# Performance work log

Measured on AMD Instinct MI355X. Metric: run time of the kernel, lower is better.

The kernel has to match this reference:

```python
import jax, jax.numpy as jnp
import numpy as np

B, N, C, H = 8, 1024, 768, 12
DH = C // H


def setup_inputs() -> dict:
    key = jax.random.key(0)
    k1, k2, k3, k4 = jax.random.split(key, 4)
    x = jax.random.normal(k1, (B, N, C), dtype=jnp.float32)
    mask = jax.random.randint(k2, (B, N), 0, 2, dtype=jnp.int32)
    # torch Linear weights stored transposed; build directly as (in, out)
    w_qkv = jax.random.normal(k3, (C, 3 * C), dtype=jnp.float32) * (C ** -0.5)
    w_proj = jax.random.normal(k4, (C, C), dtype=jnp.float32) * (C ** -0.5)
    b_proj = jnp.zeros((C,), dtype=jnp.float32)
    return {"x": x, "mask": mask, "w_qkv": w_qkv, "w_proj": w_proj, "b_proj": b_proj}


def reference(x, mask, w_qkv, w_proj, b_proj):
    scale = DH ** -0.5
    qkv = (x @ w_qkv).reshape(B, N, 3, H, DH)          # (B,N,3,H,Dh)
    q, k, v = jnp.moveaxis(qkv, 2, 0)                  # each (B,N,H,Dh)
    q = q.transpose(0, 2, 1, 3)                        # (B,H,N,Dh)
    k = k.transpose(0, 2, 1, 3)
    v = v.transpose(0, 2, 1, 3)
    attn = jnp.einsum('bhqd,bhkd->bhqk', q, k) * scale  # (B,H,N,N)
    # mask (B,N) masks key positions for all queries/heads
    attn = jnp.where(mask[:, None, None, :] != 0, -jnp.inf, attn)
    attn = jax.nn.softmax(attn, axis=-1)
    out = jnp.einsum('bhqk,bhkd->bhqd', attn, v)        # (B,H,N,Dh)
    out = out.transpose(0, 2, 1, 3).reshape(B, N, C)
    return out @ w_proj + b_proj
```

## Files before the change

### kernel.cpp

```cpp
#include <hip/hip_runtime.h>
#include <cstdint>
#include <cstddef>

#define Bb   8
#define Nn   1024
#define Ccn  768
#define Hh   12
#define DHn  64
#define Mrows (Bb * Nn)
#define N3C  (3 * Ccn)
#define BHn  (Bb * Hh)

typedef __attribute__((ext_vector_type(8))) short bf16x8;
typedef __attribute__((ext_vector_type(4))) float f32x4;

static __device__ __forceinline__ unsigned short f2bf(float f) {
    unsigned int u = __builtin_bit_cast(unsigned int, f);
    return (unsigned short)((u + 0x7FFFu + ((u >> 16) & 1u)) >> 16);
}
static __device__ __forceinline__ float bf2f(unsigned short s) {
    unsigned int u = ((unsigned int)s) << 16;
    return __builtin_bit_cast(float, u);
}
static __device__ __forceinline__ unsigned pack2bf(float a, float b) {
    unsigned ua = __builtin_bit_cast(unsigned, a) + 0x8000u;
    unsigned ub = __builtin_bit_cast(unsigned, b) + 0x8000u;
    return (ua >> 16) | (ub & 0xFFFF0000u);
}
static __device__ __forceinline__ void glds16(const void* g, void* l) {
    __builtin_amdgcn_global_load_lds((const __attribute__((address_space(1))) void*)g,
                                     (__attribute__((address_space(3))) void*)l,
                                     16, 0, 0);
}

__global__ void prep_kernel(const float* __restrict__ x,
                            unsigned short* __restrict__ xb,
                            const int* __restrict__ mask,
                            float* __restrict__ maskneg,
                            const float* __restrict__ Wqkv,
                            unsigned short* __restrict__ WqkvT,
                            const float* __restrict__ Wproj,
                            unsigned short* __restrict__ WprojT) {
    __shared__ float tile[32][33];
    int bx = blockIdx.x;
    if (bx < 3072) {
        int i = bx * 256 + threadIdx.x;
        if (i < Mrows) maskneg[i] = (mask[i] != 0) ? -1.0e9f : 0.0f;
        const f32x4* xp = (const f32x4*)x;
        f32x4 a = xp[2 * i], b = xp[2 * i + 1];
        bf16x8 v;
#pragma unroll
        for (int j = 0; j < 4; ++j) {
            v[j]     = (short)f2bf(a[j]);
            v[4 + j] = (short)f2bf(b[j]);
        }
        ((bf16x8*)xb)[i] = v;
        return;
    }
    bx -= 3072;
    int xt = bx % 96, yt = bx / 96;
    const float* W; unsigned short* WT; int C;
    if (xt < 72) { W = Wqkv;  WT = WqkvT;  C = N3C; }
    else         { W = Wproj; WT = WprojT; C = Ccn; xt -= 72; }
    const int R = Ccn;
    const int c0 = xt * 32, r0 = yt * 32;
    const int tx = threadIdx.x & 31, ty = threadIdx.x >> 5;
#pragma unroll
    for (int i = 0; i < 4; ++i)
        tile[ty + i * 8][tx] = W[(size_t)(r0 + ty + i * 8) * C + c0 + tx];
    __syncthreads();
#pragma unroll
    for (int i = 0; i < 4; ++i)
        WT[(size_t)(c0 + ty + i * 8) * R + r0 + tx] = f2bf(tile[tx][ty + i * 8]);
}

__global__ void transpose_v_kernel(const unsigned short* __restrict__ vb,
                                   unsigned short* __restrict__ vtb) {
    __shared__ unsigned short tile[32][34];
    const int bh = blockIdx.z;
    const int d0 = blockIdx.x * 32, n0 = blockIdx.y * 32;
    const int tx = threadIdx.x, ty = threadIdx.y;
    const unsigned short* src = vb + (size_t)bh * Nn * DHn;
    unsigned short* dst = vtb + (size_t)bh * DHn * Nn;
#pragma unroll
    for (int i = 0; i < 4; ++i)
        tile[ty + i * 8][tx] = src[(size_t)(n0 + ty + i * 8) * DHn + d0 + tx];
    __syncthreads();
#pragma unroll
    for (int i = 0; i < 4; ++i)
        dst[(size_t)(d0 + ty + i * 8) * Nn + n0 + tx] = tile[tx][ty + i * 8];
}

__global__ __launch_bounds__(256) void gemm_qkv_kernel(
    const unsigned short* __restrict__ A,
    const unsigned short* __restrict__ BT,
    unsigned short* __restrict__ qkvb) {
    constexpr int K = Ccn;
    const int bm = blockIdx.x, bn = blockIdx.y;
    const int t = threadIdx.x, wv = t >> 6, l = t & 63;
    const int fr = l & 15, quad = l >> 4;
    const int wm = (wv >> 1) * 64, wn = (wv & 1) * 64;
    __shared__ __align__(16) unsigned short As[2][128 * 32];
    __shared__ __align__(16) unsigned short Bs[2][128 * 32];
    const f32x4 zero = {0.f, 0.f, 0.f, 0.f};
    f32x4 acc[4][4];
#pragma unroll
    for (int i = 0; i < 4; ++i)
#pragma unroll
        for (int j = 0; j < 4; ++j) acc[i][j] = zero;

    const int srow = wv * 16 + (l >> 2);
    const int scol_dst = (l & 3) * 8;
    const int scol_src = (((l & 3) ^ ((srow >> 1) & 3)) << 3);
    const unsigned short* Ag = A + (size_t)(bm * 128 + srow) * K + scol_src;
    const unsigned short* Bg = BT + (size_t)(bn * 128 + srow) * K + scol_src;
    const int ldst = srow * 32 + scol_dst;
    const int rsw = ((fr >> 1) & 3);

    auto stage = [&](int r, int bsel) {
        const unsigned short* Ar = Ag + r * 32;
        const unsigned short* Br = Bg + r * 32;
        glds16(Ar, &As[bsel][ldst]);
        glds16(Ar + (size_t)64 * K, &As[bsel][ldst + 64 * 32]);
        glds16(Br, &Bs[bsel][ldst]);
        glds16(Br + (size_t)64 * K, &Bs[bsel][ldst + 64 * 32]);
    };
    stage(0, 0);
    __syncthreads();
    for (int r = 0; r < 24; ++r) {
        if (r < 23) stage(r + 1, (r + 1) & 1);
        const unsigned short* Asb = As[r & 1];
        const unsigned short* Bsb = Bs[r & 1];
        bf16x8 af[4], bfv[4];
#pragma unroll
        for (int i = 0; i < 4; ++i)
            af[i] = *(const bf16x8*)&Asb[(wm + i * 16 + fr) * 32 + ((quad ^ rsw) << 3)];
#pragma unroll
        for (int i = 0; i < 4; ++i)
            bfv[i] = *(const bf16x8*)&Bsb[(wn + i * 16 + fr) * 32 + ((quad ^ rsw) << 3)];
#pragma unroll
        for (int i = 0; i < 4; ++i)
#pragma unroll
            for (int j = 0; j < 4; ++j)
                acc[i][j] = __builtin_amdgcn_mfma_f32_16x16x32_bf16(af[i], bfv[j], acc[i][j], 0, 0, 0);
        __syncthreads();
    }
#pragma unroll
    for (int j = 0; j < 4; ++j) {
        int col = bn * 128 + wn + j * 16 + fr;
        int s = col / Ccn;
        int rem = col - s * Ccn;
        int hh = rem >> 6, d = rem & 63;
#pragma unroll
        for (int i = 0; i < 4; ++i) {
#pragma unroll
            for (int r = 0; r < 4; ++r) {
                int row = bm * 128 + wm + i * 16 + quad * 4 + r;
                int b = row >> 10, nq = row & 1023;
                qkvb[((((size_t)s * Bb + b) * Hh + hh) * Nn + nq) * DHn + d] = f2bf(acc[i][j][r]);
            }
        }
    }
}

__global__ __launch_bounds__(256) void gemm_proj_kernel(
    const unsigned short* __restrict__ A,
    const unsigned short* __restrict__ BT,
    const float* __restrict__ bias,
    float* __restrict__ out) {
    constexpr int K = Ccn;
    const int bm = blockIdx.x, bn = blockIdx.y;
    const int t = threadIdx.x, wv = t >> 6, l = t & 63;
    const int fr = l & 15, quad = l >> 4;
    const int wm = (wv >> 1) * 64, wn = (wv & 1) * 32;
    __shared__ __align__(16) unsigned short As[2][128 * 32];
    __shared__ __align__(16) unsigned short Bs[2][64 * 32];
    const f32x4 zero = {0.f, 0.f, 0.f, 0.f};
    f32x4 acc[4][2];
#pragma unroll
    for (int i = 0; i < 4; ++i)
#pragma unroll
        for (int j = 0; j < 2; ++j) acc[i][j] = zero;

    const int srow = wv * 16 + (l >> 2);
    const int scol_dst = (l & 3) * 8;
    const int scol_src = (((l & 3) ^ ((srow >> 1) & 3)) << 3);
    const unsigned short* Ag = A + (size_t)(bm * 128 + srow) * K + scol_src;
    const int ldstA = srow * 32 + scol_dst;
    const int rB = t >> 2, cB = t & 3;
    const int bsrc = ((cB ^ ((rB >> 1) & 3)) << 3);
    const unsigned short* Bg = BT + (size_t)(bn * 64 + rB) * K + bsrc;
    const int ldstB = rB * 32 + cB * 8;
    const int rsw = ((fr >> 1) & 3);

    auto stage = [&](int r, int bsel) {
        const unsigned short* Ar = Ag + r * 32;
        glds16(Ar, &As[bsel][ldstA]);
        glds16(Ar + (size_t)64 * K, &As[bsel][ldstA + 64 * 32]);
        glds16(Bg + r * 32, &Bs[bsel][ldstB]);
    };
    stage(0, 0);
    __syncthreads();
    for (int r = 0; r < 24; ++r) {
        if (r < 23) stage(r + 1, (r + 1) & 1);
        const unsigned short* Asb = As[r & 1];
        const unsigned short* Bsb = Bs[r & 1];
        bf16x8 af[4], bfv[2];
#pragma unroll
        for (int i = 0; i < 4; ++i)
            af[i] = *(const bf16x8*)&Asb[(wm + i * 16 + fr) * 32 + ((quad ^ rsw) << 3)];
#pragma unroll
        for (int j = 0; j < 2; ++j)
            bfv[j] = *(const bf16x8*)&Bsb[(wn + j * 16 + fr) * 32 + ((quad ^ rsw) << 3)];
#pragma unroll
        for (int i = 0; i < 4; ++i)
#pragma unroll
            for (int j = 0; j < 2; ++j)
                acc[i][j] = __builtin_amdgcn_mfma_f32_16x16x32_bf16(af[i], bfv[j], acc[i][j], 0, 0, 0);
        __syncthreads();
    }
#pragma unroll
    for (int j = 0; j < 2; ++j) {
        int col = bn * 64 + wn + j * 16 + fr;
        float bv = bias[col];
#pragma unroll
        for (int i = 0; i < 4; ++i) {
#pragma unroll
            for (int r = 0; r < 4; ++r) {
                int row = bm * 128 + wm + i * 16 + quad * 4 + r;
                out[(size_t)row * Ccn + col] = acc[i][j][r] + bv;
            }
        }
    }
}

__global__ __launch_bounds__(256, 3) void attn_fused(
    const unsigned short* __restrict__ qkvb,
    const unsigned short* __restrict__ vtb,
    const float* __restrict__ maskneg,
    unsigned short* __restrict__ attnb) {
    const int hb = blockIdx.x, qt = blockIdx.y;
    const int b = hb / Hh, h = hb - b * Hh;
    const int t = threadIdx.x, wv = t >> 6, l = t & 63;
    const int fr = l & 15, quad = l >> 4;
    __shared__ __align__(16) unsigned short Ks[2][64 * 64];
    __shared__ __align__(16) unsigned short VTs[2][64 * 64];
    __shared__ __align__(16) float Ms[2][64];
    __shared__ __align__(16) unsigned short Pbuf[4][16 * 72];
    const size_t bh = (size_t)b * Hh + h;
    const unsigned short* Qg = qkvb + bh * (Nn * DHn);
    const unsigned short* Kg = qkvb + (BHn + bh) * (Nn * DHn);
    const unsigned short* Vg = vtb + bh * (DHn * Nn);
    const float* Mg = maskneg + b * Nn;
    const int q0 = qt * 128 + wv * 32;

    bf16x8 qf[2][2];
#pragma unroll
    for (int g = 0; g < 2; ++g)
#pragma unroll
        for (int c = 0; c < 2; ++c) {
            bf16x8 raw = *(const bf16x8*)&Qg[(size_t)(q0 + g * 16 + fr) * DHn + c * 32 + quad * 8];
            bf16x8 sc;
#pragma unroll
            for (int j = 0; j < 8; ++j)
                sc[j] = (short)f2bf(bf2f((unsigned short)raw[j]) * 0.125f);
            qf[g][c] = sc;
        }
    const f32x4 zero = {0.f, 0.f, 0.f, 0.f};
    f32x4 o[2][4];
    float rs[2] = {0.f, 0.f};
#pragma unroll
    for (int g = 0; g < 2; ++g)
#pragma unroll
        for (int r = 0; r < 4; ++r) o[g][r] = zero;

    const int srow = wv * 8 + (l >> 3);
    const int lincol = (l & 7) * 8;
    const int swzcol = (((l & 7) ^ (srow & 7)) << 3);

    auto stage = [&](int kbase, int bsel) {
        glds16(&Kg[(size_t)(kbase + srow) * DHn + swzcol], &Ks[bsel][srow * 64 + lincol]);
        glds16(&Kg[(size_t)(kbase + srow + 32) * DHn + swzcol], &Ks[bsel][(srow + 32) * 64 + lincol]);
        glds16(&Vg[(size_t)srow * Nn + kbase + swzcol], &VTs[bsel][srow * 64 + lincol]);
        glds16(&Vg[(size_t)(srow + 32) * Nn + kbase + swzcol], &VTs[bsel][(srow + 32) * 64 + lincol]);
        if (t < 16) glds16(&Mg[kbase + t * 4], &Ms[bsel][t * 4]);
    };
    auto compute = [&](int bsel) {
        f32x4 ci[4];
#pragma unroll
        for (int kt = 0; kt < 4; ++kt)
            ci[kt] = *(const f32x4*)&Ms[bsel][kt * 16 + quad * 4];
        bf16x8 kf0[4], kf1[4];
#pragma unroll
        for (int kt = 0; kt < 4; ++kt) {
            int rr = kt * 16 + fr, sw = rr & 7;
            kf0[kt] = *(const bf16x8*)&Ks[bsel][rr * 64 + ((quad ^ sw) << 3)];
            kf1[kt] = *(const bf16x8*)&Ks[bsel][rr * 64 + (((quad + 4) ^ sw) << 3)];
        }
        f32x4 sg[2][4];
#pragma unroll
        for (int g = 0; g < 2; ++g)
#pragma unroll
            for (int kt = 0; kt < 4; ++kt) {
                f32x4 s = __builtin_amdgcn_mfma_f32_16x16x32_bf16(kf0[kt], qf[g][0], ci[kt], 0, 0, 0);
                sg[g][kt] = __builtin_amdgcn_mfma_f32_16x16x32_bf16(kf1[kt], qf[g][1], s, 0, 0, 0);
            }
        bf16x8 vf0[4], vf1[4];
#pragma unroll
        for (int dt = 0; dt < 4; ++dt) {
            int rr = dt * 16 + fr, sw = rr & 7;
            vf0[dt] = *(const bf16x8*)&VTs[bsel][rr * 64 + ((quad ^ sw) << 3)];
            vf1[dt] = *(const bf16x8*)&VTs[bsel][rr * 64 + (((quad + 4) ^ sw) << 3)];
        }
        unsigned short* Pw = Pbuf[wv];
#pragma unroll
        for (int g = 0; g < 2; ++g) {
#pragma unroll
            for (int kt = 0; kt < 4; ++kt) {
                float p0 = __expf(sg[g][kt][0]);
                float p1 = __expf(sg[g][kt][1]);
                float p2 = __expf(sg[g][kt][2]);
                float p3 = __expf(sg[g][kt][3]);
                rs[g] += (p0 + p1) + (p2 + p3);
                uint2 pk;
                pk.x = pack2bf(p0, p1);
                pk.y = pack2bf(p2, p3);
                *(uint2*)&Pw[fr * 72 + kt * 16 + quad * 4] = pk;
            }
            bf16x8 pa0 = *(const bf16x8*)&Pw[fr * 72 + quad * 8];
            bf16x8 pa1 = *(const bf16x8*)&Pw[fr * 72 + 32 + quad * 8];
#pragma unroll
            for (int dt = 0; dt < 4; ++dt) {
                f32x4 t0 = __builtin_amdgcn_mfma_f32_16x16x32_bf16(pa0, vf0[dt], o[g][dt], 0, 0, 0);
                o[g][dt] = __builtin_amdgcn_mfma_f32_16x16x32_bf16(pa1, vf1[dt], t0, 0, 0, 0);
            }
        }
    };

    stage(0, 0);
    __syncthreads();
    for (int r = 0; r < 16; ++r) {
        if (r < 15) stage((r + 1) * 64, (r + 1) & 1);
        compute(r & 1);
        __syncthreads();
    }
#pragma unroll
    for (int g = 0; g < 2; ++g) {
        float r2 = rs[g] + __shfl_xor(rs[g], 16, 64);
        float rfull = r2 + __shfl_xor(r2, 32, 64);
        float inv[4];
#pragma unroll
        for (int r = 0; r < 4; ++r) {
            float lv = __shfl(rfull, quad * 4 + r, 64);
            inv[r] = (lv > 0.f) ? 1.0f / lv : 0.f;
        }
#pragma unroll
        for (int dt = 0; dt < 4; ++dt)
#pragma unroll
            for (int r = 0; r < 4; ++r) {
                int q = q0 + g * 16 + quad * 4 + r;
                attnb[((size_t)(b * Nn + q) * Hh + h) * DHn + dt * 16 + fr] = f2bf(o[g][dt][r] * inv[r]);
            }
    }
}

#define OFF_XB     0u
#define OFF_WQKVT  12582912u
#define OFF_WPROJT 16121856u
#define OFF_MASKB  17301504u
#define OFF_QKVB   17334272u
#define OFF_VTB    55083008u
#define OFF_ATTNB  67665920u

extern "C" void kernel_launch(void* const* d_in, const int* in_sizes, int n_in,
                              void* d_out, int out_size, void* d_ws, size_t ws_size,
                              hipStream_t stream) {
    const float* x      = (const float*)d_in[0];
    const int*   mask   = (const int*)d_in[1];
    const float* w_qkv  = (const float*)d_in[2];
    const float* w_proj = (const float*)d_in[3];
    const float* b_proj = (const float*)d_in[4];
    float* out = (float*)d_out;
    char* ws = (char*)d_ws;
    unsigned short* xb     = (unsigned short*)(ws + OFF_XB);
    unsigned short* wqkvT  = (unsigned short*)(ws + OFF_WQKVT);
    unsigned short* wprojT = (unsigned short*)(ws + OFF_WPROJT);
    float*          maskng = (float*)(ws + OFF_MASKB);
    unsigned short* qkvb   = (unsigned short*)(ws + OFF_QKVB);
    unsigned short* vtb    = (unsigned short*)(ws + OFF_VTB);
    unsigned short* attnb  = (unsigned short*)(ws + OFF_ATTNB);

    prep_kernel<<<dim3(5376), dim3(256), 0, stream>>>(x, xb, mask, maskng,
                                                      w_qkv, wqkvT, w_proj, wprojT);
    gemm_qkv_kernel<<<dim3(Mrows / 128, N3C / 128), dim3(256), 0, stream>>>(xb, wqkvT, qkvb);
    transpose_v_kernel<<<dim3(DHn / 32, Nn / 32, BHn), dim3(32, 8), 0, stream>>>(
        qkvb + (size_t)2 * BHn * Nn * DHn, vtb);
    attn_fused<<<dim3(BHn, Nn / 128), dim3(256), 0, stream>>>(qkvb, vtb, maskng, attnb);
    gemm_proj_kernel<<<dim3(Mrows / 128, Ccn / 64), dim3(256), 0, stream>>>(attnb, wprojT, b_proj, out);
}
```

Baseline: 200.2 us.

## Replace double-buffered K=32 GEMM staging with single-buffer K=64 tiles

Both GEMM kernels (QKV and output projection) drop the two-stage double-buffered LDS pipeline with 32-wide K tiles. They now load 64-wide K tiles into a single buffer with an 8-way XOR swizzle. This halves the number of loop iterations and barriers and gives two MFMA sub-steps per tile. In exchange, global loads no longer overlap with compute within a block, so latency hiding now relies on occupancy across blocks.

```diff
diff --git a/kernel.cpp b/kernel.cpp
--- a/kernel.cpp
+++ b/kernel.cpp
@@ -100,8 +100,8 @@
     const int t = threadIdx.x, wv = t >> 6, l = t & 63;
     const int fr = l & 15, quad = l >> 4;
     const int wm = (wv >> 1) * 64, wn = (wv & 1) * 64;
-    __shared__ __align__(16) unsigned short As[2][128 * 32];
-    __shared__ __align__(16) unsigned short Bs[2][128 * 32];
+    __shared__ __align__(16) unsigned short As[128 * 64];
+    __shared__ __align__(16) unsigned short Bs[128 * 64];
     const f32x4 zero = {0.f, 0.f, 0.f, 0.f};
     f32x4 acc[4][4];
 #pragma unroll
@@ -109,40 +109,39 @@
 #pragma unroll
         for (int j = 0; j < 4; ++j) acc[i][j] = zero;
 
-    const int srow = wv * 16 + (l >> 2);
-    const int scol_dst = (l & 3) * 8;
-    const int scol_src = (((l & 3) ^ ((srow >> 1) & 3)) << 3);
-    const unsigned short* Ag = A + (size_t)(bm * 128 + srow) * K + scol_src;
-    const unsigned short* Bg = BT + (size_t)(bn * 128 + srow) * K + scol_src;
-    const int ldst = srow * 32 + scol_dst;
-    const int rsw = ((fr >> 1) & 3);
-
-    auto stage = [&](int r, int bsel) {
-        const unsigned short* Ar = Ag + r * 32;
-        const unsigned short* Br = Bg + r * 32;
-        glds16(Ar, &As[bsel][ldst]);
-        glds16(Ar + (size_t)64 * K, &As[bsel][ldst + 64 * 32]);
-        glds16(Br, &Bs[bsel][ldst]);
-        glds16(Br + (size_t)64 * K, &Bs[bsel][ldst + 64 * 32]);
-    };
-    stage(0, 0);
-    __syncthreads();
-    for (int r = 0; r < 24; ++r) {
-        if (r < 23) stage(r + 1, (r + 1) & 1);
-        const unsigned short* Asb = As[r & 1];
-        const unsigned short* Bsb = Bs[r & 1];
-        bf16x8 af[4], bfv[4];
-#pragma unroll
-        for (int i = 0; i < 4; ++i)
-            af[i] = *(const bf16x8*)&Asb[(wm + i * 16 + fr) * 32 + ((quad ^ rsw) << 3)];
-#pragma unroll
-        for (int i = 0; i < 4; ++i)
-            bfv[i] = *(const bf16x8*)&Bsb[(wn + i * 16 + fr) * 32 + ((quad ^ rsw) << 3)];
-#pragma unroll
-        for (int i = 0; i < 4; ++i)
-#pragma unroll
-            for (int j = 0; j < 4; ++j)
-                acc[i][j] = __builtin_amdgcn_mfma_f32_16x16x32_bf16(af[i], bfv[j], acc[i][j], 0, 0, 0);
+    const int srow = t >> 3;
+    const int c8 = t & 7;
+    const int lincol = c8 * 8;
+    const int swz = ((c8 ^ (srow & 7)) << 3);
+    const unsigned short* Ag = A + (size_t)(bm * 128 + srow) * K + swz;
+    const unsigned short* Bg = BT + (size_t)(bn * 128 + srow) * K + swz;
+
+    for (int k0 = 0; k0 < K; k0 += 64) {
+#pragma unroll
+        for (int hh = 0; hh < 4; ++hh) {
+            glds16(Ag + (size_t)(32 * hh) * K + k0, &As[(srow + 32 * hh) * 64 + lincol]);
+            glds16(Bg + (size_t)(32 * hh) * K + k0, &Bs[(srow + 32 * hh) * 64 + lincol]);
+        }
+        __syncthreads();
+#pragma unroll
+        for (int s = 0; s < 2; ++s) {
+            bf16x8 af[4], bfv[4];
+#pragma unroll
+            for (int i = 0; i < 4; ++i) {
+                int rr = wm + i * 16 + fr;
+                af[i] = *(const bf16x8*)&As[rr * 64 + (((s * 4 + quad) ^ (rr & 7)) << 3)];
+            }
+#pragma unroll
+            for (int j = 0; j < 4; ++j) {
+                int rr = wn + j * 16 + fr;
+                bfv[j] = *(const bf16x8*)&Bs[rr * 64 + (((s * 4 + quad) ^ (rr & 7)) << 3)];
+            }
+#pragma unroll
+            for (int i = 0; i < 4; ++i)
+#pragma unroll
+                for (int j = 0; j < 4; ++j)
+                    acc[i][j] = __builtin_amdgcn_mfma_f32_16x16x32_bf16(af[i], bfv[j], acc[i][j], 0, 0, 0);
+        }
         __syncthreads();
     }
 #pragma unroll
@@ -173,8 +172,8 @@
     const int t = threadIdx.x, wv = t >> 6, l = t & 63;
     const int fr = l & 15, quad = l >> 4;
     const int wm = (wv >> 1) * 64, wn = (wv & 1) * 32;
-    __shared__ __align__(16) unsigned short As[2][128 * 32];
-    __shared__ __align__(16) unsigned short Bs[2][64 * 32];
+    __shared__ __align__(16) unsigned short As[128 * 64];
+    __shared__ __align__(16) unsigned short Bs[64 * 64];
     const f32x4 zero = {0.f, 0.f, 0.f, 0.f};
     f32x4 acc[4][2];
 #pragma unroll
@@ -182,41 +181,40 @@
 #pragma unroll
         for (int j = 0; j < 2; ++j) acc[i][j] = zero;
 
-    const int srow = wv * 16 + (l >> 2);
-    const int scol_dst = (l & 3) * 8;
-    const int scol_src = (((l & 3) ^ ((srow >> 1) & 3)) << 3);
-    const unsigned short* Ag = A + (size_t)(bm * 128 + srow) * K + scol_src;
-    const int ldstA = srow * 32 + scol_dst;
-    const int rB = t >> 2, cB = t & 3;
-    const int bsrc = ((cB ^ ((rB >> 1) & 3)) << 3);
-    const unsigned short* Bg = BT + (size_t)(bn * 64 + rB) * K + bsrc;
-    const int ldstB = rB * 32 + cB * 8;
-    const int rsw = ((fr >> 1) & 3);
-
-    auto stage = [&](int r, int bsel) {
-        const unsigned short* Ar = Ag + r * 32;
-        glds16(Ar, &As[bsel][ldstA]);
-        glds16(Ar + (size_t)64 * K, &As[bsel][ldstA + 64 * 32]);
-        glds16(Bg + r * 32, &Bs[bsel][ldstB]);
-    };
-    stage(0, 0);
-    __syncthreads();
-    for (int r = 0; r < 24; ++r) {
-        if (r < 23) stage(r + 1, (r + 1) & 1);
-        const unsigned short* Asb = As[r & 1];
-        const unsigned short* Bsb = Bs[r & 1];
-        bf16x8 af[4], bfv[2];
-#pragma unroll
-        for (int i = 0; i < 4; ++i)
-            af[i] = *(const bf16x8*)&Asb[(wm + i * 16 + fr) * 32 + ((quad ^ rsw) << 3)];
-#pragma unroll
-        for (int j = 0; j < 2; ++j)
-            bfv[j] = *(const bf16x8*)&Bsb[(wn + j * 16 + fr) * 32 + ((quad ^ rsw) << 3)];
-#pragma unroll
-        for (int i = 0; i < 4; ++i)
-#pragma unroll
-            for (int j = 0; j < 2; ++j)
-                acc[i][j] = __builtin_amdgcn_mfma_f32_16x16x32_bf16(af[i], bfv[j], acc[i][j], 0, 0, 0);
+    const int srow = t >> 3;
+    const int c8 = t & 7;
+    const int lincol = c8 * 8;
+    const int swz = ((c8 ^ (srow & 7)) << 3);
+    const unsigned short* Ag = A + (size_t)(bm * 128 + srow) * K + swz;
+    const unsigned short* Bg = BT + (size_t)(bn * 64 + srow) * K + swz;
+
+    for (int k0 = 0; k0 < K; k0 += 64) {
+#pragma unroll
+        for (int hh = 0; hh < 4; ++hh)
+            glds16(Ag + (size_t)(32 * hh) * K + k0, &As[(srow + 32 * hh) * 64 + lincol]);
+#pragma unroll
+        for (int hh = 0; hh < 2; ++hh)
+            glds16(Bg + (size_t)(32 * hh) * K + k0, &Bs[(srow + 32 * hh) * 64 + lincol]);
+        __syncthreads();
+#pragma unroll
+        for (int s = 0; s < 2; ++s) {
+            bf16x8 af[4], bfv[2];
+#pragma unroll
+            for (int i = 0; i < 4; ++i) {
+                int rr = wm + i * 16 + fr;
+                af[i] = *(const bf16x8*)&As[rr * 64 + (((s * 4 + quad) ^ (rr & 7)) << 3)];
+            }
+#pragma unroll
+            for (int j = 0; j < 2; ++j) {
+                int rr = wn + j * 16 + fr;
+                bfv[j] = *(const bf16x8*)&Bs[rr * 64 + (((s * 4 + quad) ^ (rr & 7)) << 3)];
+            }
+#pragma unroll
+            for (int i = 0; i < 4; ++i)
+#pragma unroll
+                for (int j = 0; j < 2; ++j)
+                    acc[i][j] = __builtin_amdgcn_mfma_f32_16x16x32_bf16(af[i], bfv[j], acc[i][j], 0, 0, 0);
+        }
         __syncthreads();
     }
 #pragma unroll
```

New measurement: 193.8 us. 3.2% less time.
